# Kernel optimization log

Measured on AMD Instinct MI355X. Metric: run time of the kernel, lower is better.

Reference implementation:

```python
import jax, jax.numpy as jnp
import numpy as np

N_NODES = 20000
N_EDGES = 320000
DIM_IN = 768
DIM_H = 512
S_HOPS = 3
NUM_GNNS = 4
NEG_SLOPE = 0.2  # DGL GATConv default


def setup_inputs() -> dict:
    key = jax.random.key(0)
    ks = jax.random.split(key, 12)
    feat = jax.random.normal(ks[0], (N_NODES, DIM_IN), dtype=jnp.float32)
    src = jax.random.randint(ks[1], (N_EDGES,), 0, N_NODES)
    dst = jax.random.randint(ks[2], (N_EDGES,), 0, N_NODES)
    # learned params
    fc_W = jax.random.normal(ks[3], (DIM_IN, DIM_H), dtype=jnp.float32) * 0.02
    fc_b = jnp.zeros((DIM_H,), dtype=jnp.float32)
    gat_W = jax.random.normal(ks[4], (NUM_GNNS, DIM_H, DIM_H), dtype=jnp.float32) * 0.02
    gat_al = jax.random.normal(ks[5], (NUM_GNNS, DIM_H), dtype=jnp.float32) * 0.1
    gat_ar = jax.random.normal(ks[6], (NUM_GNNS, DIM_H), dtype=jnp.float32) * 0.1
    gat_b = jnp.zeros((NUM_GNNS, DIM_H), dtype=jnp.float32)
    beta = jnp.ones((S_HOPS + 1,), dtype=jnp.float32)
    return {"feat": feat, "fc_W": fc_W, "fc_b": fc_b, "gat_W": gat_W,
            "gat_al": gat_al, "gat_ar": gat_ar, "gat_b": gat_b,
            "beta": beta, "src": src, "dst": dst}


def _gat_layer(h, W, a_l, a_r, b, src, dst):
    z = h @ W                                   # [N, DH]
    el = z @ a_l                                # [N]
    er = z @ a_r                                # [N]
    e = jax.nn.leaky_relu(el[src] + er[dst], NEG_SLOPE)  # [E]
    # edge softmax over incoming edges of each dst node
    m = jax.ops.segment_max(e, dst, num_segments=N_NODES)
    ex = jnp.exp(e - m[dst])
    denom = jax.ops.segment_sum(ex, dst, num_segments=N_NODES)
    alpha = ex / denom[dst]                     # [E]
    out = jax.ops.segment_sum(alpha[:, None] * z[src], dst, num_segments=N_NODES)
    return out + b


def reference(feat, fc_W, fc_b, gat_W, gat_al, gat_ar, gat_b, beta, src, dst):
    h = feat @ fc_W + fc_b                      # dim_in -> 512
    for l in range(NUM_GNNS):
        h = _gat_layer(h, gat_W[l], gat_al[l], gat_ar[l], gat_b[l], src, dst)
    # A_hat = A + I propagation; A_hat @ Z = scatter(Z[src] -> dst) + Z
    Z_prev = h
    Z = beta[0] * Z_prev                        # accumulated Z is computed but the
    for s in range(1, S_HOPS + 1):              # original module returns Z_prev
        Z_s = jax.ops.segment_sum(Z_prev[src], dst, num_segments=N_NODES) + Z_prev
        Z = Z + beta[s] * Z_s
        Z_prev = Z_s
    return Z_prev
```

## Files before the change

kernel.cpp:

```cpp
#include <hip/hip_runtime.h>
#include <math.h>

#define N_NODES 20000
#define M_PAD   20096
#define N_EDGES 320000
#define DIM_IN 768
#define DIM_H 512
#define NUM_GNNS 4
#define NEG_SLOPE 0.2f

#define GEMM_TILES 628
#define GEMM_GRID  632

#define SLC_GRID 5000

typedef __attribute__((ext_vector_type(8))) short short8;
typedef __attribute__((ext_vector_type(4))) float f32x4;

#define GPTR(p) (const __attribute__((address_space(1))) void*)(p)
#define LPTR(p) (__attribute__((address_space(3))) void*)(p)

__device__ __forceinline__ float bf2f(unsigned int lo16) {
  return __uint_as_float(lo16 << 16);
}
__device__ __forceinline__ unsigned short f2bf(float f) {
  unsigned int u = __float_as_uint(f);
  u += 0x7FFFu + ((u >> 16) & 1u);
  return (unsigned short)(u >> 16);
}
__device__ __forceinline__ void unpack8(uint4 v, float* f) {
  f[0] = bf2f(v.x & 0xffffu); f[1] = bf2f(v.x >> 16);
  f[2] = bf2f(v.y & 0xffffu); f[3] = bf2f(v.y >> 16);
  f[4] = bf2f(v.z & 0xffffu); f[5] = bf2f(v.z >> 16);
  f[6] = bf2f(v.w & 0xffffu); f[7] = bf2f(v.w >> 16);
}
__device__ __forceinline__ uint4 pack8(const float* o) {
  uint4 pv;
  pv.x = (unsigned)f2bf(o[0]) | ((unsigned)f2bf(o[1]) << 16);
  pv.y = (unsigned)f2bf(o[2]) | ((unsigned)f2bf(o[3]) << 16);
  pv.z = (unsigned)f2bf(o[4]) | ((unsigned)f2bf(o[5]) << 16);
  pv.w = (unsigned)f2bf(o[6]) | ((unsigned)f2bf(o[7]) << 16);
  return pv;
}

__device__ __forceinline__ float waveReduceSum(float v) {
#pragma unroll
  for (int off = 32; off > 0; off >>= 1) v += __shfl_xor(v, off, 64);
  return v;
}
__device__ __forceinline__ float waveReduceMax(float v) {
#pragma unroll
  for (int off = 32; off > 0; off >>= 1) v = fmaxf(v, __shfl_xor(v, off, 64));
  return v;
}

__global__ __launch_bounds__(256) void gemm_mfma_bf16(
    const unsigned short* __restrict__ A,
    const unsigned short* __restrict__ Bt,
    const float* __restrict__ bias,
    unsigned short* __restrict__ Cbf,
    int K) {
  int bid = blockIdx.x;
  int tile = (bid & 7) * (GEMM_GRID / 8) + (bid >> 3);
  if (tile >= GEMM_TILES) return;
  int brow = tile >> 2;
  int bcol = tile & 3;

  __shared__ __align__(16) unsigned short lds[4][128 * 32];
  int tid = threadIdx.x;
  int wave = tid >> 6, lane = tid & 63;
  int wm = wave >> 1, wn = wave & 1;

  int rl = lane >> 2;
  int kc = (lane & 3) ^ ((lane >> 3) & 3);
  int r0 = 32 * wave;
  const unsigned short* gA0 = A + (size_t)(brow * 128 + r0 + rl) * K + kc * 8;
  const unsigned short* gA1 = gA0 + (size_t)16 * K;
  const unsigned short* gB0 = Bt + (size_t)(bcol * 128 + r0 + rl) * K + kc * 8;
  const unsigned short* gB1 = gB0 + (size_t)16 * K;

  int mrow = lane & 15;
  int q = lane >> 4;
  int swz = (q ^ ((mrow >> 1) & 3)) * 8;

  f32x4 acc[4][4];
#pragma unroll
  for (int i = 0; i < 4; ++i)
#pragma unroll
    for (int j = 0; j < 4; ++j) acc[i][j] = (f32x4)(0.f);

  int nk = K >> 5;
  {
    unsigned short* lA = lds[0] + r0 * 32;
    unsigned short* lB = lds[2] + r0 * 32;
    __builtin_amdgcn_global_load_lds(GPTR(gA0), LPTR(lA), 16, 0, 0);
    __builtin_amdgcn_global_load_lds(GPTR(gA1), LPTR(lA + 512), 16, 0, 0);
    __builtin_amdgcn_global_load_lds(GPTR(gB0), LPTR(lB), 16, 0, 0);
    __builtin_amdgcn_global_load_lds(GPTR(gB1), LPTR(lB + 512), 16, 0, 0);
  }
  __syncthreads();

  for (int t = 0; t < nk; ++t) {
    int cur = t & 1;
    if (t + 1 < nk) {
      int k0 = (t + 1) << 5;
      unsigned short* lA = lds[cur ^ 1] + r0 * 32;
      unsigned short* lB = lds[2 + (cur ^ 1)] + r0 * 32;
      __builtin_amdgcn_global_load_lds(GPTR(gA0 + k0), LPTR(lA), 16, 0, 0);
      __builtin_amdgcn_global_load_lds(GPTR(gA1 + k0), LPTR(lA + 512), 16, 0, 0);
      __builtin_amdgcn_global_load_lds(GPTR(gB0 + k0), LPTR(lB), 16, 0, 0);
      __builtin_amdgcn_global_load_lds(GPTR(gB1 + k0), LPTR(lB + 512), 16, 0, 0);
    }
    const short8* ra = (const short8*)(lds[cur] + (64 * wm + mrow) * 32 + swz);
    const short8* rb = (const short8*)(lds[2 + cur] + (64 * wn + mrow) * 32 + swz);
    short8 a[4], b[4];
#pragma unroll
    for (int u = 0; u < 4; ++u) a[u] = ra[u * 64];
#pragma unroll
    for (int u = 0; u < 4; ++u) b[u] = rb[u * 64];
#pragma unroll
    for (int mt = 0; mt < 4; ++mt)
#pragma unroll
      for (int nt = 0; nt < 4; ++nt)
        acc[mt][nt] = __builtin_amdgcn_mfma_f32_16x16x32_bf16(a[mt], b[nt], acc[mt][nt], 0, 0, 0);
    __syncthreads();
  }

  unsigned short* Cs = lds[0];
  {
    float bv[4];
#pragma unroll
    for (int nt = 0; nt < 4; ++nt)
      bv[nt] = bias ? bias[bcol * 128 + 64 * wn + 16 * nt + mrow] : 0.f;
#pragma unroll
    for (int mt = 0; mt < 4; ++mt)
#pragma unroll
      for (int nt = 0; nt < 4; ++nt)
#pragma unroll
        for (int i = 0; i < 4; ++i) {
          int row = 64 * wm + 16 * mt + 4 * q + i;
          int col = 64 * wn + 16 * nt + mrow;
          Cs[row * 128 + col] = f2bf(acc[mt][nt][i] + bv[nt]);
        }
  }
  __syncthreads();
  int rr = tid >> 4, cb = (tid & 15) * 8;
#pragma unroll
  for (int it = 0; it < 8; ++it, rr += 16) {
    uint4 val = *(const uint4*)(Cs + rr * 128 + cb);
    *(uint4*)(Cbf + (size_t)(brow * 128 + rr) * DIM_H + bcol * 128 + cb) = val;
  }
}

__global__ void convert_feat(const float* __restrict__ feat, unsigned short* __restrict__ Abf) {
  int t = blockIdx.x * blockDim.x + threadIdx.x;
  const int CHUNKS = M_PAD * DIM_IN / 8;
  if (t >= CHUNKS) return;
  int row = t / (DIM_IN / 8);
  uint4 o;
  if (row < N_NODES) {
    const float4* p = (const float4*)(feat + (size_t)t * 8);
    float4 x = p[0], y = p[1];
    o.x = (unsigned)f2bf(x.x) | ((unsigned)f2bf(x.y) << 16);
    o.y = (unsigned)f2bf(x.z) | ((unsigned)f2bf(x.w) << 16);
    o.z = (unsigned)f2bf(y.x) | ((unsigned)f2bf(y.y) << 16);
    o.w = (unsigned)f2bf(y.z) | ((unsigned)f2bf(y.w) << 16);
  } else {
    o = make_uint4(0, 0, 0, 0);
  }
  ((uint4*)Abf)[t] = o;
}

__global__ __launch_bounds__(256) void transpose_bf16(const float* __restrict__ in,
                                                      unsigned short* __restrict__ out,
                                                      int R, int C) {
  __shared__ float tile[32][33];
  int tx = threadIdx.x, ty = threadIdx.y;
  size_t base = (size_t)blockIdx.z * R * C;
  int r0 = blockIdx.x * 32, c0 = blockIdx.y * 32;
#pragma unroll
  for (int i = 0; i < 4; ++i) {
    int r = r0 + ty + i * 8;
    tile[ty + i * 8][tx] = in[base + (size_t)r * C + c0 + tx];
  }
  __syncthreads();
#pragma unroll
  for (int i = 0; i < 4; ++i) {
    int c = c0 + ty + i * 8;
    out[base + (size_t)c * R + r0 + tx] = f2bf(tile[tx][ty + i * 8]);
  }
}

__global__ void count_edges(const int* __restrict__ dst, int* __restrict__ counts) {
  int k = blockIdx.x * blockDim.x + threadIdx.x;
  if (k < N_EDGES) atomicAdd(&counts[dst[k]], 1);
}

__global__ __launch_bounds__(1024) void scan_kernel(const int* __restrict__ counts,
                                                    int* __restrict__ indptr) {
  __shared__ int part[1024];
  int tid = threadIdx.x;
  const int CH = (N_NODES + 1023) / 1024;
  int base = tid * CH;
  int s = 0;
  for (int i = 0; i < CH; ++i) {
    int idx = base + i;
    if (idx < N_NODES) s += counts[idx];
  }
  part[tid] = s;
  __syncthreads();
  for (int off = 1; off < 1024; off <<= 1) {
    int v = (tid >= off) ? part[tid - off] : 0;
    __syncthreads();
    part[tid] += v;
    __syncthreads();
  }
  int run = (tid == 0) ? 0 : part[tid - 1];
  for (int i = 0; i < CH; ++i) {
    int idx = base + i;
    if (idx < N_NODES) {
      indptr[idx] = run;
      run += counts[idx];
      if (idx == N_NODES - 1) indptr[N_NODES] = run;
    }
  }
}

__global__ void fill_adj(const int* __restrict__ src, const int* __restrict__ dst,
                         const int* __restrict__ indptr, int* __restrict__ cursor,
                         int* __restrict__ adjsrc) {
  int k = blockIdx.x * blockDim.x + threadIdx.x;
  if (k < N_EDGES) {
    int d = dst[k];
    int pos = atomicAdd(&cursor[d], 1);
    adjsrc[indptr[d] + pos] = src[k];
  }
}

__global__ void pack_ones(const int* __restrict__ adjsrc, int2* __restrict__ apairs) {
  int k = blockIdx.x * blockDim.x + threadIdx.x;
  if (k < N_EDGES) apairs[k] = make_int2(adjsrc[k], __float_as_int(1.0f));
}

__global__ __launch_bounds__(256) void eler_bf(const unsigned short* __restrict__ zbf,
                                               const float* __restrict__ al,
                                               const float* __restrict__ ar,
                                               float* __restrict__ el, float* __restrict__ er) {
  int wid = (blockIdx.x * blockDim.x + threadIdx.x) >> 6;
  int lane = threadIdx.x & 63;
  if (wid >= N_NODES) return;
  uint4 zv = ((const uint4*)(zbf + (size_t)wid * DIM_H))[lane];
  float z[8];
  unpack8(zv, z);
  const float4* al4 = (const float4*)(al + lane * 8);
  const float4* ar4 = (const float4*)(ar + lane * 8);
  float4 a0 = al4[0], a1 = al4[1], r0 = ar4[0], r1 = ar4[1];
  float sl = z[0] * a0.x + z[1] * a0.y + z[2] * a0.z + z[3] * a0.w +
             z[4] * a1.x + z[5] * a1.y + z[6] * a1.z + z[7] * a1.w;
  float sr = z[0] * r0.x + z[1] * r0.y + z[2] * r0.z + z[3] * r0.w +
             z[4] * r1.x + z[5] * r1.y + z[6] * r1.z + z[7] * r1.w;
  sl = waveReduceSum(sl);
  sr = waveReduceSum(sr);
  if (lane == 0) { el[wid] = sl; er[wid] = sr; }
}

__global__ __launch_bounds__(256) void edge_softmax_alpha(
    const float* __restrict__ el, const float* __restrict__ er,
    const int* __restrict__ indptr, const int* __restrict__ adjsrc,
    float* __restrict__ alpha, int2* __restrict__ apairs) {
  int v = (blockIdx.x * blockDim.x + threadIdx.x) >> 6;
  int lane = threadIdx.x & 63;
  if (v >= N_NODES) return;
  int begin = indptr[v], end = indptr[v + 1];
  float er_v = er[v];

  float m = -INFINITY;
  for (int j = begin + lane; j < end; j += 64) {
    float e = el[adjsrc[j]] + er_v;
    e = (e >= 0.f) ? e : NEG_SLOPE * e;
    alpha[j] = e;
    m = fmaxf(m, e);
  }
  m = waveReduceMax(m);

  float ss = 0.f;
  for (int j = begin + lane; j < end; j += 64) {
    float ex = __expf(alpha[j] - m);
    alpha[j] = ex;
    ss += ex;
  }
  float denom = waveReduceSum(ss);
  float inv = (end > begin) ? 1.f / denom : 0.f;

  for (int j = begin + lane; j < end; j += 64)
    apairs[j] = make_int2(adjsrc[j], __float_as_int(alpha[j] * inv));
}

__global__ __launch_bounds__(256) void gather_slc(
    const unsigned short* __restrict__ zin, const int2* __restrict__ apairs,
    const int* __restrict__ indptr, const float* __restrict__ bias, int self_term,
    unsigned short* __restrict__ out_bf, float* __restrict__ out_f32) {
  int slice = blockIdx.x & 7;
  int grp = blockIdx.x >> 3;
  int wave = threadIdx.x >> 6, lane = threadIdx.x & 63;
  int slot = lane >> 3, sub = lane & 7;
  int v = grp * 32 + wave * 8 + slot;
  unsigned cbyte = (unsigned)(slice * 128 + sub * 16);
  const char* zb = (const char*)zin;
  const char* pb = (const char*)apairs;

  int b = indptr[v];
  int deg = indptr[v + 1] - b;
  int md = deg;
  md = max(md, __shfl_xor(md, 8, 64));
  md = max(md, __shfl_xor(md, 16, 64));
  md = max(md, __shfl_xor(md, 32, 64));

  float acc[8];
  if (self_term) {
    uint4 sz = *(const uint4*)(zb + (((unsigned)v) << 10) + cbyte);
    unpack8(sz, acc);
  } else {
#pragma unroll
    for (int i = 0; i < 8; ++i) acc[i] = 0.f;
  }

  const unsigned NMAX = (unsigned)(N_NODES - 1);
  unsigned ab = ((unsigned)b) << 3;
  int2 ra[8];
#pragma unroll
  for (int u = 0; u < 8; ++u) ra[u] = *(const int2*)(pb + ab + u * 8);
#pragma nounroll
  for (int t = 0; t < md; t += 8) {
    int2 rn[8];
    if (t + 8 < md) {
#pragma unroll
      for (int u = 0; u < 8; ++u) rn[u] = *(const int2*)(pb + ab + 64 + u * 8);
    } else {
#pragma unroll
      for (int u = 0; u < 8; ++u) rn[u] = ra[u];
    }
    int rem = deg - t;
#pragma unroll
    for (int u = 0; u < 8; ++u) {
      unsigned uidx = min((unsigned)ra[u].x, NMAX);
      float wv = (u < rem) ? __int_as_float(ra[u].y) : 0.f;
      uint4 z = *(const uint4*)(zb + (uidx << 10) + cbyte);
      float f[8];
      unpack8(z, f);
#pragma unroll
      for (int i = 0; i < 8; ++i) acc[i] = fmaf(wv, f[i], acc[i]);
    }
#pragma unroll
    for (int u = 0; u < 8; ++u) ra[u] = rn[u];
    ab += 64;
  }

  if (bias) {
    const float4* b4 = (const float4*)(bias + slice * 64 + sub * 8);
    float4 b0 = b4[0], b1 = b4[1];
    acc[0] += b0.x; acc[1] += b0.y; acc[2] += b0.z; acc[3] += b0.w;
    acc[4] += b1.x; acc[5] += b1.y; acc[6] += b1.z; acc[7] += b1.w;
  }
  if (out_bf) {
    uint4 pv = pack8(acc);
    *(uint4*)((char*)out_bf + (((unsigned)v) << 10) + cbyte) = pv;
  } else {
    char* p = (char*)out_f32 + (((unsigned)v) << 11) + cbyte * 2;
    *(f32x4*)p = (f32x4){acc[0], acc[1], acc[2], acc[3]};
    *(f32x4*)(p + 16) = (f32x4){acc[4], acc[5], acc[6], acc[7]};
  }
}

extern "C" void kernel_launch(void* const* d_in, const int* in_sizes, int n_in,
                              void* d_out, int out_size, void* d_ws, size_t ws_size,
                              hipStream_t stream) {
  const float* feat = (const float*)d_in[0];
  const float* fc_W = (const float*)d_in[1];
  const float* fc_b = (const float*)d_in[2];
  const float* gat_W = (const float*)d_in[3];
  const float* gat_al = (const float*)d_in[4];
  const float* gat_ar = (const float*)d_in[5];
  const float* gat_b = (const float*)d_in[6];
  const int* src = (const int*)d_in[8];
  const int* dst = (const int*)d_in[9];
  float* out = (float*)d_out;

  char* w = (char*)d_ws;
  auto alloc = [&](size_t bytes) {
    char* p = w;
    w += (bytes + 255) & ~(size_t)255;
    return p;
  };
  unsigned short* hbf   = (unsigned short*)alloc((size_t)M_PAD * DIM_H * 2);
  unsigned short* fcWt  = (unsigned short*)alloc((size_t)DIM_H * DIM_IN * 2);
  unsigned short* gatWt = (unsigned short*)alloc((size_t)NUM_GNNS * DIM_H * DIM_H * 2);
  float* el    = (float*)alloc((size_t)N_NODES * 4);
  float* er    = (float*)alloc((size_t)N_NODES * 4);
  int* counts  = (int*)alloc((size_t)2 * N_NODES * 4);
  int* cursor  = counts + N_NODES;
  int* indptr  = (int*)alloc((size_t)(N_NODES + 1) * 4);
  int* adjsrc  = (int*)alloc((size_t)(N_EDGES + 64) * 4);
  char* uni = alloc((size_t)M_PAD * DIM_IN * 2);
  unsigned short* Abf = (unsigned short*)uni;
  float* alpha = (float*)uni;
  unsigned short* Z1  = (unsigned short*)uni;
  int2* apairs = (int2*)(uni + (size_t)M_PAD * DIM_H * 2);
  unsigned short* zbf = (unsigned short*)d_out;

  hipMemsetAsync(counts, 0, sizeof(int) * 2 * N_NODES, stream);
  count_edges<<<(N_EDGES + 255) / 256, 256, 0, stream>>>(dst, counts);
  scan_kernel<<<1, 1024, 0, stream>>>(counts, indptr);
  fill_adj<<<(N_EDGES + 255) / 256, 256, 0, stream>>>(src, dst, indptr, cursor, adjsrc);

  convert_feat<<<(M_PAD * DIM_IN / 8 + 255) / 256, 256, 0, stream>>>(feat, Abf);
  transpose_bf16<<<dim3(DIM_IN / 32, DIM_H / 32, 1), dim3(32, 8), 0, stream>>>(fc_W, fcWt, DIM_IN, DIM_H);
  transpose_bf16<<<dim3(DIM_H / 32, DIM_H / 32, NUM_GNNS), dim3(32, 8), 0, stream>>>(gat_W, gatWt, DIM_H, DIM_H);

  gemm_mfma_bf16<<<GEMM_GRID, 256, 0, stream>>>(Abf, fcWt, fc_b, hbf, DIM_IN);

  int nwaveblocks = (N_NODES * 64 + 255) / 256;
  for (int l = 0; l < NUM_GNNS; ++l) {
    gemm_mfma_bf16<<<GEMM_GRID, 256, 0, stream>>>(hbf, gatWt + (size_t)l * DIM_H * DIM_H,
                                                  nullptr, zbf, DIM_H);
    eler_bf<<<nwaveblocks, 256, 0, stream>>>(zbf, gat_al + (size_t)l * DIM_H,
                                             gat_ar + (size_t)l * DIM_H, el, er);
    edge_softmax_alpha<<<nwaveblocks, 256, 0, stream>>>(el, er, indptr, adjsrc, alpha, apairs);
    gather_slc<<<SLC_GRID, 256, 0, stream>>>(
        zbf, apairs, indptr, gat_b + (size_t)l * DIM_H, 0, hbf, nullptr);
  }

  pack_ones<<<(N_EDGES + 255) / 256, 256, 0, stream>>>(adjsrc, apairs);
  gather_slc<<<SLC_GRID, 256, 0, stream>>>(hbf, apairs, indptr, nullptr, 1, Z1, nullptr);
  gather_slc<<<SLC_GRID, 256, 0, stream>>>(Z1, apairs, indptr, nullptr, 1, hbf, nullptr);
  gather_slc<<<SLC_GRID, 256, 0, stream>>>(hbf, apairs, indptr, nullptr, 1, nullptr, out);
}
```

Baseline: 581.7 us.

## Shrink GEMM tiles to 128x64 and degree-sort nodes within gather windows

The GEMM switches from 128x128 output tiles to 128x64 tiles, doubling the grid to 1256 blocks. Each wave now computes 32x64 instead of 64x64, which improves CU fill across the grid at the cost of more B reloads and lower MFMA reuse per tile. Separately, a new kernel sorts nodes by degree within each 256-node window and writes a permutation. The gather kernel uses it so the 8 nodes sharing a wave have similar degrees, which reduces lane idling caused by degree imbalance. The cost is one extra indirection load per node.

```diff
diff --git a/kernel.cpp b/kernel.cpp
--- a/kernel.cpp
+++ b/kernel.cpp
@@ -9,8 +9,8 @@
 #define NUM_GNNS 4
 #define NEG_SLOPE 0.2f
 
-#define GEMM_TILES 628
-#define GEMM_GRID  632
+#define GEMM_TILES 1256
+#define GEMM_GRID  1256
 
 #define SLC_GRID 5000
 
@@ -62,41 +62,35 @@
     int K) {
   int bid = blockIdx.x;
   int tile = (bid & 7) * (GEMM_GRID / 8) + (bid >> 3);
-  if (tile >= GEMM_TILES) return;
-  int brow = tile >> 2;
-  int bcol = tile & 3;
-
-  __shared__ __align__(16) unsigned short lds[4][128 * 32];
+  int brow = tile >> 3;
+  int bcol = tile & 7;
+
+  __shared__ __align__(16) unsigned short As[2][128 * 32];
+  __shared__ __align__(16) unsigned short Bs[2][64 * 32];
   int tid = threadIdx.x;
   int wave = tid >> 6, lane = tid & 63;
-  int wm = wave >> 1, wn = wave & 1;
 
   int rl = lane >> 2;
   int kc = (lane & 3) ^ ((lane >> 3) & 3);
-  int r0 = 32 * wave;
-  const unsigned short* gA0 = A + (size_t)(brow * 128 + r0 + rl) * K + kc * 8;
+  const unsigned short* gA0 = A + (size_t)(brow * 128 + 32 * wave + rl) * K + kc * 8;
   const unsigned short* gA1 = gA0 + (size_t)16 * K;
-  const unsigned short* gB0 = Bt + (size_t)(bcol * 128 + r0 + rl) * K + kc * 8;
-  const unsigned short* gB1 = gB0 + (size_t)16 * K;
+  const unsigned short* gB0 = Bt + (size_t)(bcol * 64 + 16 * wave + rl) * K + kc * 8;
 
   int mrow = lane & 15;
   int q = lane >> 4;
   int swz = (q ^ ((mrow >> 1) & 3)) * 8;
 
-  f32x4 acc[4][4];
-#pragma unroll
-  for (int i = 0; i < 4; ++i)
+  f32x4 acc[2][4];
+#pragma unroll
+  for (int i = 0; i < 2; ++i)
 #pragma unroll
     for (int j = 0; j < 4; ++j) acc[i][j] = (f32x4)(0.f);
 
   int nk = K >> 5;
   {
-    unsigned short* lA = lds[0] + r0 * 32;
-    unsigned short* lB = lds[2] + r0 * 32;
-    __builtin_amdgcn_global_load_lds(GPTR(gA0), LPTR(lA), 16, 0, 0);
-    __builtin_amdgcn_global_load_lds(GPTR(gA1), LPTR(lA + 512), 16, 0, 0);
-    __builtin_amdgcn_global_load_lds(GPTR(gB0), LPTR(lB), 16, 0, 0);
-    __builtin_amdgcn_global_load_lds(GPTR(gB1), LPTR(lB + 512), 16, 0, 0);
+    __builtin_amdgcn_global_load_lds(GPTR(gA0), LPTR(As[0] + 32 * wave * 32), 16, 0, 0);
+    __builtin_amdgcn_global_load_lds(GPTR(gA1), LPTR(As[0] + (32 * wave + 16) * 32), 16, 0, 0);
+    __builtin_amdgcn_global_load_lds(GPTR(gB0), LPTR(Bs[0] + 16 * wave * 32), 16, 0, 0);
   }
   __syncthreads();
 
@@ -104,51 +98,49 @@
     int cur = t & 1;
     if (t + 1 < nk) {
       int k0 = (t + 1) << 5;
-      unsigned short* lA = lds[cur ^ 1] + r0 * 32;
-      unsigned short* lB = lds[2 + (cur ^ 1)] + r0 * 32;
-      __builtin_amdgcn_global_load_lds(GPTR(gA0 + k0), LPTR(lA), 16, 0, 0);
-      __builtin_amdgcn_global_load_lds(GPTR(gA1 + k0), LPTR(lA + 512), 16, 0, 0);
-      __builtin_amdgcn_global_load_lds(GPTR(gB0 + k0), LPTR(lB), 16, 0, 0);
-      __builtin_amdgcn_global_load_lds(GPTR(gB1 + k0), LPTR(lB + 512), 16, 0, 0);
+      int nxt = cur ^ 1;
+      __builtin_amdgcn_global_load_lds(GPTR(gA0 + k0), LPTR(As[nxt] + 32 * wave * 32), 16, 0, 0);
+      __builtin_amdgcn_global_load_lds(GPTR(gA1 + k0), LPTR(As[nxt] + (32 * wave + 16) * 32), 16, 0, 0);
+      __builtin_amdgcn_global_load_lds(GPTR(gB0 + k0), LPTR(Bs[nxt] + 16 * wave * 32), 16, 0, 0);
     }
-    const short8* ra = (const short8*)(lds[cur] + (64 * wm + mrow) * 32 + swz);
-    const short8* rb = (const short8*)(lds[2 + cur] + (64 * wn + mrow) * 32 + swz);
-    short8 a[4], b[4];
-#pragma unroll
-    for (int u = 0; u < 4; ++u) a[u] = ra[u * 64];
+    const short8* ra = (const short8*)(As[cur] + (32 * wave + mrow) * 32 + swz);
+    const short8* rb = (const short8*)(Bs[cur] + mrow * 32 + swz);
+    short8 a[2], b[4];
+#pragma unroll
+    for (int u = 0; u < 2; ++u) a[u] = ra[u * 64];
 #pragma unroll
     for (int u = 0; u < 4; ++u) b[u] = rb[u * 64];
 #pragma unroll
-    for (int mt = 0; mt < 4; ++mt)
+    for (int mt = 0; mt < 2; ++mt)
 #pragma unroll
       for (int nt = 0; nt < 4; ++nt)
         acc[mt][nt] = __builtin_amdgcn_mfma_f32_16x16x32_bf16(a[mt], b[nt], acc[mt][nt], 0, 0, 0);
     __syncthreads();
   }
 
-  unsigned short* Cs = lds[0];
+  unsigned short* Cs = &As[0][0];
   {
     float bv[4];
 #pragma unroll
     for (int nt = 0; nt < 4; ++nt)
-      bv[nt] = bias ? bias[bcol * 128 + 64 * wn + 16 * nt + mrow] : 0.f;
-#pragma unroll
-    for (int mt = 0; mt < 4; ++mt)
+      bv[nt] = bias ? bias[bcol * 64 + 16 * nt + mrow] : 0.f;
+#pragma unroll
+    for (int mt = 0; mt < 2; ++mt)
 #pragma unroll
       for (int nt = 0; nt < 4; ++nt)
 #pragma unroll
         for (int i = 0; i < 4; ++i) {
-          int row = 64 * wm + 16 * mt + 4 * q + i;
-          int col = 64 * wn + 16 * nt + mrow;
-          Cs[row * 128 + col] = f2bf(acc[mt][nt][i] + bv[nt]);
+          int row = 32 * wave + 16 * mt + 4 * q + i;
+          int col = 16 * nt + mrow;
+          Cs[row * 64 + col] = f2bf(acc[mt][nt][i] + bv[nt]);
         }
   }
   __syncthreads();
-  int rr = tid >> 4, cb = (tid & 15) * 8;
-#pragma unroll
-  for (int it = 0; it < 8; ++it, rr += 16) {
-    uint4 val = *(const uint4*)(Cs + rr * 128 + cb);
-    *(uint4*)(Cbf + (size_t)(brow * 128 + rr) * DIM_H + bcol * 128 + cb) = val;
+  int rr = tid >> 3, cb = (tid & 7) * 8;
+#pragma unroll
+  for (int it = 0; it < 4; ++it, rr += 32) {
+    uint4 val = *(const uint4*)(Cs + rr * 64 + cb);
+    *(uint4*)(Cbf + (size_t)(brow * 128 + rr) * DIM_H + bcol * 64 + cb) = val;
   }
 }
 
@@ -234,6 +226,34 @@
     int d = dst[k];
     int pos = atomicAdd(&cursor[d], 1);
     adjsrc[indptr[d] + pos] = src[k];
+  }
+}
+
+__global__ __launch_bounds__(256) void build_perm_win(const int* __restrict__ counts,
+                                                      int* __restrict__ perm) {
+  __shared__ int hist[64];
+  __shared__ int basec[64];
+  int tid = threadIdx.x;
+  int v0 = blockIdx.x * 256;
+  int n = min(256, N_NODES - v0);
+  if (tid < 64) hist[tid] = 0;
+  __syncthreads();
+  int deg = 0, b = 0;
+  if (tid < n) {
+    deg = counts[v0 + tid];
+    b = min(deg, 63);
+    atomicAdd(&hist[b], 1);
+  }
+  __syncthreads();
+  if (tid == 0) {
+    int run = 0;
+#pragma unroll
+    for (int i = 0; i < 64; ++i) { basec[i] = run; run += hist[i]; }
+  }
+  __syncthreads();
+  if (tid < n) {
+    int pos = atomicAdd(&basec[b], 1);
+    perm[v0 + pos] = v0 + tid;
   }
 }
 
@@ -298,13 +318,15 @@
 
 __global__ __launch_bounds__(256) void gather_slc(
     const unsigned short* __restrict__ zin, const int2* __restrict__ apairs,
-    const int* __restrict__ indptr, const float* __restrict__ bias, int self_term,
+    const int* __restrict__ indptr, const int* __restrict__ perm,
+    const float* __restrict__ bias, int self_term,
     unsigned short* __restrict__ out_bf, float* __restrict__ out_f32) {
   int slice = blockIdx.x & 7;
   int grp = blockIdx.x >> 3;
   int wave = threadIdx.x >> 6, lane = threadIdx.x & 63;
   int slot = lane >> 3, sub = lane & 7;
-  int v = grp * 32 + wave * 8 + slot;
+  int vidx = grp * 32 + wave * 8 + slot;
+  int v = perm[vidx];
   unsigned cbyte = (unsigned)(slice * 128 + sub * 16);
   const char* zb = (const char*)zin;
   const char* pb = (const char*)apairs;
@@ -401,6 +423,7 @@
   int* cursor  = counts + N_NODES;
   int* indptr  = (int*)alloc((size_t)(N_NODES + 1) * 4);
   int* adjsrc  = (int*)alloc((size_t)(N_EDGES + 64) * 4);
+  int* perm    = (int*)alloc((size_t)N_NODES * 4);
   char* uni = alloc((size_t)M_PAD * DIM_IN * 2);
   unsigned short* Abf = (unsigned short*)uni;
   float* alpha = (float*)uni;
@@ -412,6 +435,7 @@
   count_edges<<<(N_EDGES + 255) / 256, 256, 0, stream>>>(dst, counts);
   scan_kernel<<<1, 1024, 0, stream>>>(counts, indptr);
   fill_adj<<<(N_EDGES + 255) / 256, 256, 0, stream>>>(src, dst, indptr, cursor, adjsrc);
+  build_perm_win<<<(N_NODES + 255) / 256, 256, 0, stream>>>(counts, perm);
 
   convert_feat<<<(M_PAD * DIM_IN / 8 + 255) / 256, 256, 0, stream>>>(feat, Abf);
   transpose_bf16<<<dim3(DIM_IN / 32, DIM_H / 32, 1), dim3(32, 8), 0, stream>>>(fc_W, fcWt, DIM_IN, DIM_H);
@@ -427,11 +451,11 @@
                                              gat_ar + (size_t)l * DIM_H, el, er);
     edge_softmax_alpha<<<nwaveblocks, 256, 0, stream>>>(el, er, indptr, adjsrc, alpha, apairs);
     gather_slc<<<SLC_GRID, 256, 0, stream>>>(
-        zbf, apairs, indptr, gat_b + (size_t)l * DIM_H, 0, hbf, nullptr);
+        zbf, apairs, indptr, perm, gat_b + (size_t)l * DIM_H, 0, hbf, nullptr);
   }
 
   pack_ones<<<(N_EDGES + 255) / 256, 256, 0, stream>>>(adjsrc, apairs);
-  gather_slc<<<SLC_GRID, 256, 0, stream>>>(hbf, apairs, indptr, nullptr, 1, Z1, nullptr);
-  gather_slc<<<SLC_GRID, 256, 0, stream>>>(Z1, apairs, indptr, nullptr, 1, hbf, nullptr);
-  gather_slc<<<SLC_GRID, 256, 0, stream>>>(hbf, apairs, indptr, nullptr, 1, nullptr, out);
-}
+  gather_slc<<<SLC_GRID, 256, 0, stream>>>(hbf, apairs, indptr, perm, nullptr, 1, Z1, nullptr);
+  gather_slc<<<SLC_GRID, 256, 0, stream>>>(Z1, apairs, indptr, perm, nullptr, 1, hbf, nullptr);
+  gather_slc<<<SLC_GRID, 256, 0, stream>>>(hbf, apairs, indptr, perm, nullptr, 1, nullptr, out);
+}
```

Measured after the change: 590.8 us. Within noise of the previous version (+1.6%).
